# Kernel optimization log

Measured on AMD Instinct MI355X. Metric: run time of the kernel, lower is better.

Reference implementation:

```python
import jax, jax.numpy as jnp
import numpy as np

N = 100000
E = 1600000
IN_C = 64
HID = 64


def sage_conv(x, edge_index, W_l, b_l, W_r):
    # PyG SAGEConv with mean aggregation:
    # out = lin_l(mean_{j in N(i)} x_j) + lin_r(x_i)
    src, dst = edge_index[0], edge_index[1]
    msgs = x[src]                                        # [E, C] gather
    summed = jax.ops.segment_sum(msgs, dst, num_segments=N)   # [N, C]
    count = jax.ops.segment_sum(jnp.ones((edge_index.shape[1],), x.dtype), dst,
                                num_segments=N)          # [N]
    agg = summed / jnp.maximum(count, 1.0)[:, None]      # mean, safe for isolated nodes
    return agg @ W_l + b_l + x @ W_r


def setup_inputs() -> dict:
    key = jax.random.key(0)
    ks = jax.random.split(key, 10)
    x = jax.random.normal(ks[0], (N, IN_C), dtype=jnp.float32)
    edge_index = jax.random.randint(ks[1], (2, E), 0, N, dtype=jnp.int64)
    s1 = 1.0 / np.sqrt(IN_C)
    s2 = 1.0 / np.sqrt(HID)
    W_l1 = jax.random.uniform(ks[2], (IN_C, HID), jnp.float32, -s1, s1)
    b_l1 = jax.random.uniform(ks[3], (HID,), jnp.float32, -s1, s1)
    W_r1 = jax.random.uniform(ks[4], (IN_C, HID), jnp.float32, -s1, s1)
    W_l2 = jax.random.uniform(ks[5], (HID, HID), jnp.float32, -s2, s2)
    b_l2 = jax.random.uniform(ks[6], (HID,), jnp.float32, -s2, s2)
    W_r2 = jax.random.uniform(ks[7], (HID, HID), jnp.float32, -s2, s2)
    W_c = jax.random.uniform(ks[8], (HID, 1), jnp.float32, -s2, s2)
    b_c = jax.random.uniform(ks[9], (1,), jnp.float32, -s2, s2)
    return {"x": x, "edge_index": edge_index,
            "W_l1": W_l1, "b_l1": b_l1, "W_r1": W_r1,
            "W_l2": W_l2, "b_l2": b_l2, "W_r2": W_r2,
            "W_c": W_c, "b_c": b_c}


def reference(x, edge_index, W_l1, b_l1, W_r1, W_l2, b_l2, W_r2, W_c, b_c):
    h = jax.nn.relu(sage_conv(x, edge_index, W_l1, b_l1, W_r1))
    # dropout p=0.2 is identity in eval mode
    h = jax.nn.relu(sage_conv(h, edge_index, W_l2, b_l2, W_r2))
    out = (h @ W_c + b_c).squeeze(-1)   # [N]
    return out
```

## Files before the change

kernel.cpp:

```cpp
#include <hip/hip_runtime.h>


#define C 64
#define NB 196
#define BCAP 16000

typedef _Float16 half8 __attribute__((ext_vector_type(8)));
typedef float f32x4 __attribute__((ext_vector_type(4)));

static inline size_t align256(size_t x) { return (x + 255) & ~(size_t)255; }

__device__ void cvt_part(const float* __restrict__ x, _Float16* __restrict__ xh,
                         int n8, int bid) {
    int i = bid * 256 + (int)threadIdx.x;
    if (i < n8) {
        const float4* p = (const float4*)x + (size_t)i * 2;
        float4 a = p[0], b = p[1];
        half8 h;
        h[0] = (_Float16)a.x; h[1] = (_Float16)a.y; h[2] = (_Float16)a.z; h[3] = (_Float16)a.w;
        h[4] = (_Float16)b.x; h[5] = (_Float16)b.y; h[6] = (_Float16)b.z; h[7] = (_Float16)b.w;
        ((half8*)xh)[i] = h;
    }
}

__device__ void wpack_part(const float* __restrict__ W0, const float* __restrict__ W1,
                           const float* __restrict__ W2, const float* __restrict__ W3,
                           _Float16* __restrict__ wp, int bid) {
    int t = bid * 256 + (int)threadIdx.x;
    if (t >= 2048) return;
    int lane = t & 63, step = (t >> 6) & 1, tile = (t >> 7) & 3, mat = t >> 9;
    const float* W = (mat == 0) ? W0 : (mat == 1) ? W1 : (mat == 2) ? W2 : W3;
    int col = tile * 16 + (lane & 15);
    int k0  = step * 32 + ((lane >> 4) << 3);
    half8 h;
    #pragma unroll
    for (int j = 0; j < 8; ++j) h[j] = (_Float16)W[(k0 + j) * C + col];
    ((half8*)wp)[t] = h;
}

__global__ __launch_bounds__(256) void prep2_kernel(
    const float* __restrict__ x, _Float16* __restrict__ xh, int n8,
    const float* __restrict__ W0, const float* __restrict__ W1,
    const float* __restrict__ W2, const float* __restrict__ W3,
    _Float16* __restrict__ wp, int cgrid)
{
    int bid = blockIdx.x;
    if (bid < cgrid) cvt_part(x, xh, n8, bid);
    else             wpack_part(W0, W1, W2, W3, wp, bid - cgrid);
}

__global__ __launch_bounds__(256) void bucket1_kernel(
    const int* __restrict__ ei, int* __restrict__ bucketCnt,
    unsigned* __restrict__ records, int E)
{
    __shared__ int cnt[NB], cur[NB], gbase[NB];
    const int t = (int)threadIdx.x;
    for (int b = t; b < NB; b += 256) { cnt[b] = 0; cur[b] = 0; }
    __syncthreads();
    const int nE4 = E >> 2;
    const int base4 = blockIdx.x * 1024;
    #pragma unroll
    for (int j = 0; j < 4; ++j) {
        int i4 = base4 + j * 256 + t;
        if (i4 < nE4) {
            int4 d = ((const int4*)(ei + E))[i4];
            atomicAdd(&cnt[d.x >> 9], 1);
            atomicAdd(&cnt[d.y >> 9], 1);
            atomicAdd(&cnt[d.z >> 9], 1);
            atomicAdd(&cnt[d.w >> 9], 1);
        }
    }
    __syncthreads();
    for (int b = t; b < NB; b += 256)
        gbase[b] = cnt[b] ? atomicAdd(&bucketCnt[b], cnt[b]) : 0;
    __syncthreads();
    #pragma unroll
    for (int j = 0; j < 4; ++j) {
        int i4 = base4 + j * 256 + t;
        if (i4 < nE4) {
            int4 s = ((const int4*)ei)[i4];
            int4 d = ((const int4*)(ei + E))[i4];
            int b0 = d.x >> 9, b1 = d.y >> 9, b2 = d.z >> 9, b3 = d.w >> 9;
            int k0 = gbase[b0] + atomicAdd(&cur[b0], 1);
            int k1 = gbase[b1] + atomicAdd(&cur[b1], 1);
            int k2 = gbase[b2] + atomicAdd(&cur[b2], 1);
            int k3 = gbase[b3] + atomicAdd(&cur[b3], 1);
            if (k0 < BCAP) records[(size_t)b0 * BCAP + k0] = ((unsigned)s.x << 9) | (unsigned)(d.x & 511);
            if (k1 < BCAP) records[(size_t)b1 * BCAP + k1] = ((unsigned)s.y << 9) | (unsigned)(d.y & 511);
            if (k2 < BCAP) records[(size_t)b2 * BCAP + k2] = ((unsigned)s.z << 9) | (unsigned)(d.z & 511);
            if (k3 < BCAP) records[(size_t)b3 * BCAP + k3] = ((unsigned)s.w << 9) | (unsigned)(d.w & 511);
        }
    }
}

__global__ __launch_bounds__(256) void bucketscan_kernel(
    const int* __restrict__ bucketCnt, int* __restrict__ bucketBase,
    int* __restrict__ offs, int n)
{
    __shared__ int wsum[4];
    const int t = (int)threadIdx.x, lane = t & 63, wid = t >> 6;
    int v = (t < NB) ? min(bucketCnt[t], BCAP) : 0;
    int s = v;
    #pragma unroll
    for (int off = 1; off < 64; off <<= 1) {
        int u = __shfl_up(s, off, 64);
        if (lane >= off) s += u;
    }
    if (lane == 63) wsum[wid] = s;
    __syncthreads();
    int wpre = 0;
    for (int w = 0; w < wid; ++w) wpre += wsum[w];
    if (t < NB) bucketBase[t] = wpre + (s - v);
    if (t == 0) offs[n] = wsum[0] + wsum[1] + wsum[2] + wsum[3];
}

__global__ __launch_bounds__(256) void csrbuild_kernel(
    const unsigned* __restrict__ records, const int* __restrict__ bucketCnt,
    const int* __restrict__ bucketBase, int* __restrict__ offs,
    int* __restrict__ csr, int n)
{
    __shared__ int histo[512], cur[512], lofs[512], wsum[4];
    const int b = blockIdx.x, t = (int)threadIdx.x;
    const int cnt = min(bucketCnt[b], BCAP);
    const int bb = bucketBase[b];
    histo[t] = 0; histo[t + 256] = 0;
    cur[t] = 0;   cur[t + 256] = 0;
    __syncthreads();
    const unsigned* rec = records + (size_t)b * BCAP;
    for (int j = t; j < cnt; j += 256)
        atomicAdd(&histo[rec[j] & 511], 1);
    __syncthreads();
    int h0 = histo[2 * t], h1 = histo[2 * t + 1];
    int s = h0 + h1;
    const int lane = t & 63, wid = t >> 6;
    int si = s;
    #pragma unroll
    for (int off = 1; off < 64; off <<= 1) {
        int u = __shfl_up(si, off, 64);
        if (lane >= off) si += u;
    }
    if (lane == 63) wsum[wid] = si;
    __syncthreads();
    int wpre = 0;
    for (int w = 0; w < wid; ++w) wpre += wsum[w];
    int ex = wpre + (si - s);
    lofs[2 * t] = ex;
    lofs[2 * t + 1] = ex + h0;
    int node0 = b * 512 + 2 * t;
    if (node0 < n)     offs[node0]     = bb + ex;
    if (node0 + 1 < n) offs[node0 + 1] = bb + ex + h0;
    __syncthreads();
    for (int j = t; j < cnt; j += 256) {
        unsigned r = rec[j];
        int d = (int)(r & 511u);
        int rk = atomicAdd(&cur[d], 1);
        csr[bb + lofs[d] + rk] = (int)(r >> 9);
    }
}

template <bool FINAL>
__global__ __launch_bounds__(256) void sage_kernel(
    const _Float16* __restrict__ Xh, const int* __restrict__ csr,
    const int* __restrict__ offs,
    const _Float16* __restrict__ wpL, const _Float16* __restrict__ wpR,
    const float* __restrict__ bl,
    const float* __restrict__ Wc, const float* __restrict__ bc,
    void* __restrict__ outp, int n)
{
    const int lane = threadIdx.x & 63;
    const int wid  = threadIdx.x >> 6;
    const int base = blockIdx.x * 32;
    __shared__ _Float16 Aagg[32][72];
    __shared__ float Opart[2][2][16];

    const int slot = lane >> 3;
    const int sub  = lane & 7;
    const int node = base + wid * 8 + slot;
    float acc[8] = {0.f,0.f,0.f,0.f,0.f,0.f,0.f,0.f};
    int dcount = 0;
    if (node < n) {
        int start = offs[node];
        dcount = offs[node + 1] - start;
        int k = 0;
        for (; k + 4 <= dcount; k += 4) {
            int i0 = csr[start + k + 0];
            int i1 = csr[start + k + 1];
            int i2 = csr[start + k + 2];
            int i3 = csr[start + k + 3];
            half8 v0 = *(const half8*)(Xh + ((size_t)i0 << 6) + (sub << 3));
            half8 v1 = *(const half8*)(Xh + ((size_t)i1 << 6) + (sub << 3));
            half8 v2 = *(const half8*)(Xh + ((size_t)i2 << 6) + (sub << 3));
            half8 v3 = *(const half8*)(Xh + ((size_t)i3 << 6) + (sub << 3));
            #pragma unroll
            for (int j = 0; j < 8; ++j) acc[j] += (float)v0[j];
            #pragma unroll
            for (int j = 0; j < 8; ++j) acc[j] += (float)v1[j];
            #pragma unroll
            for (int j = 0; j < 8; ++j) acc[j] += (float)v2[j];
            #pragma unroll
            for (int j = 0; j < 8; ++j) acc[j] += (float)v3[j];
        }
        for (; k < dcount; ++k) {
            int i0 = csr[start + k];
            half8 v0 = *(const half8*)(Xh + ((size_t)i0 << 6) + (sub << 3));
            #pragma unroll
            for (int j = 0; j < 8; ++j) acc[j] += (float)v0[j];
        }
    }
    float inv = 1.0f / fmaxf((float)dcount, 1.0f);
    half8 hv;
    #pragma unroll
    for (int j = 0; j < 8; ++j) hv[j] = (_Float16)(acc[j] * inv);
    *(half8*)&Aagg[wid * 8 + slot][sub * 8] = hv;
    __syncthreads();

    const int Mtile = wid >> 1;
    const int pair  = wid & 1;
    const int row16 = lane & 15;
    const int kg    = lane >> 4;
    const int myrow = base + Mtile * 16 + row16;
    const int srow  = (myrow < n) ? myrow : 0;

    half8 ag0 = *(const half8*)&Aagg[Mtile * 16 + row16][kg * 8];
    half8 ag1 = *(const half8*)&Aagg[Mtile * 16 + row16][32 + kg * 8];
    const _Float16* xrow = Xh + ((size_t)srow << 6);
    half8 xi0 = *(const half8*)(xrow + kg * 8);
    half8 xi1 = *(const half8*)(xrow + 32 + kg * 8);

    float ptot[4] = {0.f, 0.f, 0.f, 0.f};
    #pragma unroll
    for (int q = 0; q < 2; ++q) {
        const int ct = pair * 2 + q;
        const half8* BL = (const half8*)(wpL + (size_t)ct * 1024);
        const half8* BR = (const half8*)(wpR + (size_t)ct * 1024);
        half8 b0 = BL[lane];
        half8 b1 = BL[64 + lane];
        half8 b2 = BR[lane];
        half8 b3 = BR[64 + lane];
        f32x4 cacc = {0.f, 0.f, 0.f, 0.f};
        cacc = __builtin_amdgcn_mfma_f32_16x16x32_f16(ag0, b0, cacc, 0, 0, 0);
        cacc = __builtin_amdgcn_mfma_f32_16x16x32_f16(ag1, b1, cacc, 0, 0, 0);
        cacc = __builtin_amdgcn_mfma_f32_16x16x32_f16(xi0, b2, cacc, 0, 0, 0);
        cacc = __builtin_amdgcn_mfma_f32_16x16x32_f16(xi1, b3, cacc, 0, 0, 0);

        const int col = ct * 16 + row16;
        const float bias = bl[col];
        if (!FINAL) {
            _Float16* h1 = (_Float16*)outp;
            #pragma unroll
            for (int j = 0; j < 4; ++j) {
                int r = base + Mtile * 16 + kg * 4 + j;
                if (r < n) {
                    float v = fmaxf(cacc[j] + bias, 0.f);
                    h1[((size_t)r << 6) + col] = (_Float16)v;
                }
            }
        } else {
            const float wc = Wc[col];
            float p[4];
            #pragma unroll
            for (int j = 0; j < 4; ++j) p[j] = fmaxf(cacc[j] + bias, 0.f) * wc;
            #pragma unroll
            for (int off = 1; off < 16; off <<= 1) {
                #pragma unroll
                for (int j = 0; j < 4; ++j) p[j] += __shfl_xor(p[j], off, 64);
            }
            #pragma unroll
            for (int j = 0; j < 4; ++j) ptot[j] += p[j];
        }
    }

    if (FINAL) {
        if (row16 == 0) {
            #pragma unroll
            for (int j = 0; j < 4; ++j) Opart[Mtile][pair][kg * 4 + j] = ptot[j];
        }
        __syncthreads();
        const int tid = threadIdx.x;
        if (tid < 32) {
            int Mt = tid >> 4, r = tid & 15;
            int gr = base + Mt * 16 + r;
            if (gr < n)
                ((float*)outp)[gr] = Opart[Mt][0][r] + Opart[Mt][1][r] + bc[0];
        }
    }
}

extern "C" void kernel_launch(void* const* d_in, const int* in_sizes, int n_in,
                              void* d_out, int out_size, void* d_ws, size_t ws_size,
                              hipStream_t stream) {
    const float* x   = (const float*)d_in[0];
    const int*   ei  = (const int*)d_in[1];
    const float* Wl1 = (const float*)d_in[2];
    const float* bl1 = (const float*)d_in[3];
    const float* Wr1 = (const float*)d_in[4];
    const float* Wl2 = (const float*)d_in[5];
    const float* bl2 = (const float*)d_in[6];
    const float* Wr2 = (const float*)d_in[7];
    const float* Wc  = (const float*)d_in[8];
    const float* bc  = (const float*)d_in[9];
    float* out = (float*)d_out;

    const int N = in_sizes[0] / C;
    const int E = in_sizes[1] / 2;

    char* ws = (char*)d_ws;
    size_t off = 0;
    int* offs       = (int*)(ws + off); off += align256((size_t)(N + 1) * 4);
    int* bucketCnt  = (int*)(ws + off); off += align256((size_t)NB * 4);
    int* bucketBase = (int*)(ws + off); off += align256((size_t)NB * 4);
    int* csr        = (int*)(ws + off); off += align256((size_t)E * 4);
    size_t h1_sz = (size_t)N * C * 2;
    size_t rec_sz = (size_t)NB * BCAP * 4;
    _Float16* h1 = (_Float16*)(ws + off); off += align256(h1_sz > rec_sz ? h1_sz : rec_sz);
    _Float16* xh = (_Float16*)(ws + off); off += align256((size_t)N * C * 2);
    _Float16* wp = (_Float16*)(ws + off); off += align256((size_t)2048 * 8 * 2);
    if (off > ws_size) return;

    unsigned* records = (unsigned*)h1;

    const int blk = 256;
    const int n8 = N * C / 8;
    const int cgrid = (n8 + blk - 1) / blk;
    const int nE4 = E >> 2;
    const int b1grid = (nE4 + 1023) / 1024;

    hipMemsetAsync(bucketCnt, 0, (size_t)NB * 4, stream);
    prep2_kernel<<<cgrid + 8, blk, 0, stream>>>(x, xh, n8, Wl1, Wr1, Wl2, Wr2, wp, cgrid);
    bucket1_kernel<<<b1grid, blk, 0, stream>>>(ei, bucketCnt, records, E);
    bucketscan_kernel<<<1, blk, 0, stream>>>(bucketCnt, bucketBase, offs, N);
    csrbuild_kernel<<<NB, blk, 0, stream>>>(records, bucketCnt, bucketBase, offs, csr, N);

    const int node_grid = (N + 31) / 32;
    sage_kernel<false><<<node_grid, blk, 0, stream>>>(
        xh, csr, offs, wp, wp + 4096, bl1, nullptr, nullptr, h1, N);
    sage_kernel<true><<<node_grid, blk, 0, stream>>>(
        h1, csr, offs, wp + 8192, wp + 12288, bl2, Wc, bc, out, N);
}
```

Before: 206.5 us.

## Fuse bucketing into prep kernel, fold bucket scan into CSR build, unroll gather by 8

Merges the edge-bucketing pass with the fp16 conversion and weight-packing blocks into one launch. The single-block bucket-offset scan is removed: each CSR-build block recomputes the prefix over all bucket counts itself. The destination indices are kept in registers between the count and scatter phases instead of being reloaded. The aggregation loop gains an 8-wide unrolled gather to keep more loads in flight, at the cost of register pressure and some redundant scan work in every CSR block.

```diff
diff --git a/kernel.cpp b/kernel.cpp
--- a/kernel.cpp
+++ b/kernel.cpp
@@ -9,6 +9,50 @@
 typedef float f32x4 __attribute__((ext_vector_type(4)));
 
 static inline size_t align256(size_t x) { return (x + 255) & ~(size_t)255; }
+
+__device__ void bucket1_part(const int* __restrict__ ei, int* __restrict__ bucketCnt,
+                             unsigned* __restrict__ records, int E, int bid) {
+    __shared__ int cnt[NB], cur[NB], gbase[NB];
+    const int t = (int)threadIdx.x;
+    for (int b = t; b < NB; b += 256) { cnt[b] = 0; cur[b] = 0; }
+    __syncthreads();
+    const int nE4 = E >> 2;
+    const int base4 = bid * 1024;
+    int4 dreg[4];
+    #pragma unroll
+    for (int j = 0; j < 4; ++j) {
+        int i4 = base4 + j * 256 + t;
+        if (i4 < nE4) {
+            int4 d = ((const int4*)(ei + E))[i4];
+            dreg[j] = d;
+            atomicAdd(&cnt[d.x >> 9], 1);
+            atomicAdd(&cnt[d.y >> 9], 1);
+            atomicAdd(&cnt[d.z >> 9], 1);
+            atomicAdd(&cnt[d.w >> 9], 1);
+        }
+    }
+    __syncthreads();
+    for (int b = t; b < NB; b += 256)
+        gbase[b] = cnt[b] ? atomicAdd(&bucketCnt[b], cnt[b]) : 0;
+    __syncthreads();
+    #pragma unroll
+    for (int j = 0; j < 4; ++j) {
+        int i4 = base4 + j * 256 + t;
+        if (i4 < nE4) {
+            int4 s = ((const int4*)ei)[i4];
+            int4 d = dreg[j];
+            int b0 = d.x >> 9, b1 = d.y >> 9, b2 = d.z >> 9, b3 = d.w >> 9;
+            int k0 = gbase[b0] + atomicAdd(&cur[b0], 1);
+            int k1 = gbase[b1] + atomicAdd(&cur[b1], 1);
+            int k2 = gbase[b2] + atomicAdd(&cur[b2], 1);
+            int k3 = gbase[b3] + atomicAdd(&cur[b3], 1);
+            if (k0 < BCAP) records[(size_t)b0 * BCAP + k0] = ((unsigned)s.x << 9) | (unsigned)(d.x & 511);
+            if (k1 < BCAP) records[(size_t)b1 * BCAP + k1] = ((unsigned)s.y << 9) | (unsigned)(d.y & 511);
+            if (k2 < BCAP) records[(size_t)b2 * BCAP + k2] = ((unsigned)s.z << 9) | (unsigned)(d.z & 511);
+            if (k3 < BCAP) records[(size_t)b3 * BCAP + k3] = ((unsigned)s.w << 9) | (unsigned)(d.w & 511);
+        }
+    }
+}
 
 __device__ void cvt_part(const float* __restrict__ x, _Float16* __restrict__ xh,
                          int n8, int bid) {
@@ -38,112 +82,65 @@
     ((half8*)wp)[t] = h;
 }
 
-__global__ __launch_bounds__(256) void prep2_kernel(
+__global__ __launch_bounds__(256) void prep_kernel(
+    const int* __restrict__ ei, int* __restrict__ bucketCnt,
+    unsigned* __restrict__ records, int E,
     const float* __restrict__ x, _Float16* __restrict__ xh, int n8,
     const float* __restrict__ W0, const float* __restrict__ W1,
     const float* __restrict__ W2, const float* __restrict__ W3,
-    _Float16* __restrict__ wp, int cgrid)
+    _Float16* __restrict__ wp, int bgrid, int cgrid)
 {
     int bid = blockIdx.x;
-    if (bid < cgrid) cvt_part(x, xh, n8, bid);
-    else             wpack_part(W0, W1, W2, W3, wp, bid - cgrid);
-}
-
-__global__ __launch_bounds__(256) void bucket1_kernel(
-    const int* __restrict__ ei, int* __restrict__ bucketCnt,
-    unsigned* __restrict__ records, int E)
+    if (bid < bgrid)              bucket1_part(ei, bucketCnt, records, E, bid);
+    else if (bid < bgrid + cgrid) cvt_part(x, xh, n8, bid - bgrid);
+    else                          wpack_part(W0, W1, W2, W3, wp, bid - bgrid - cgrid);
+}
+
+__global__ __launch_bounds__(256) void csrbuild_kernel(
+    const unsigned* __restrict__ records, const int* __restrict__ bucketCnt,
+    int* __restrict__ offs, int* __restrict__ csr, int n)
 {
-    __shared__ int cnt[NB], cur[NB], gbase[NB];
-    const int t = (int)threadIdx.x;
-    for (int b = t; b < NB; b += 256) { cnt[b] = 0; cur[b] = 0; }
-    __syncthreads();
-    const int nE4 = E >> 2;
-    const int base4 = blockIdx.x * 1024;
-    #pragma unroll
-    for (int j = 0; j < 4; ++j) {
-        int i4 = base4 + j * 256 + t;
-        if (i4 < nE4) {
-            int4 d = ((const int4*)(ei + E))[i4];
-            atomicAdd(&cnt[d.x >> 9], 1);
-            atomicAdd(&cnt[d.y >> 9], 1);
-            atomicAdd(&cnt[d.z >> 9], 1);
-            atomicAdd(&cnt[d.w >> 9], 1);
-        }
-    }
-    __syncthreads();
-    for (int b = t; b < NB; b += 256)
-        gbase[b] = cnt[b] ? atomicAdd(&bucketCnt[b], cnt[b]) : 0;
-    __syncthreads();
-    #pragma unroll
-    for (int j = 0; j < 4; ++j) {
-        int i4 = base4 + j * 256 + t;
-        if (i4 < nE4) {
-            int4 s = ((const int4*)ei)[i4];
-            int4 d = ((const int4*)(ei + E))[i4];
-            int b0 = d.x >> 9, b1 = d.y >> 9, b2 = d.z >> 9, b3 = d.w >> 9;
-            int k0 = gbase[b0] + atomicAdd(&cur[b0], 1);
-            int k1 = gbase[b1] + atomicAdd(&cur[b1], 1);
-            int k2 = gbase[b2] + atomicAdd(&cur[b2], 1);
-            int k3 = gbase[b3] + atomicAdd(&cur[b3], 1);
-            if (k0 < BCAP) records[(size_t)b0 * BCAP + k0] = ((unsigned)s.x << 9) | (unsigned)(d.x & 511);
-            if (k1 < BCAP) records[(size_t)b1 * BCAP + k1] = ((unsigned)s.y << 9) | (unsigned)(d.y & 511);
-            if (k2 < BCAP) records[(size_t)b2 * BCAP + k2] = ((unsigned)s.z << 9) | (unsigned)(d.z & 511);
-            if (k3 < BCAP) records[(size_t)b3 * BCAP + k3] = ((unsigned)s.w << 9) | (unsigned)(d.w & 511);
-        }
-    }
-}
-
-__global__ __launch_bounds__(256) void bucketscan_kernel(
-    const int* __restrict__ bucketCnt, int* __restrict__ bucketBase,
-    int* __restrict__ offs, int n)
-{
-    __shared__ int wsum[4];
-    const int t = (int)threadIdx.x, lane = t & 63, wid = t >> 6;
+    __shared__ int histo[512], cur[512], lofs[512], wsum[4];
+    __shared__ int bb_sh;
+    const int b = blockIdx.x, t = (int)threadIdx.x;
+    const int lane = t & 63, wid = t >> 6;
+    histo[t] = 0; histo[t + 256] = 0;
+    cur[t] = 0;   cur[t + 256] = 0;
     int v = (t < NB) ? min(bucketCnt[t], BCAP) : 0;
-    int s = v;
+    int si = v;
     #pragma unroll
     for (int off = 1; off < 64; off <<= 1) {
-        int u = __shfl_up(s, off, 64);
-        if (lane >= off) s += u;
-    }
-    if (lane == 63) wsum[wid] = s;
+        int u = __shfl_up(si, off, 64);
+        if (lane >= off) si += u;
+    }
+    if (lane == 63) wsum[wid] = si;
     __syncthreads();
     int wpre = 0;
     for (int w = 0; w < wid; ++w) wpre += wsum[w];
-    if (t < NB) bucketBase[t] = wpre + (s - v);
-    if (t == 0) offs[n] = wsum[0] + wsum[1] + wsum[2] + wsum[3];
-}
-
-__global__ __launch_bounds__(256) void csrbuild_kernel(
-    const unsigned* __restrict__ records, const int* __restrict__ bucketCnt,
-    const int* __restrict__ bucketBase, int* __restrict__ offs,
-    int* __restrict__ csr, int n)
-{
-    __shared__ int histo[512], cur[512], lofs[512], wsum[4];
-    const int b = blockIdx.x, t = (int)threadIdx.x;
+    if (t == b) bb_sh = wpre + (si - v);
+    if (b == 0 && t == 0)
+        offs[n] = wsum[0] + wsum[1] + wsum[2] + wsum[3];
+    __syncthreads();
     const int cnt = min(bucketCnt[b], BCAP);
-    const int bb = bucketBase[b];
-    histo[t] = 0; histo[t + 256] = 0;
-    cur[t] = 0;   cur[t + 256] = 0;
-    __syncthreads();
+    const int bb = bb_sh;
     const unsigned* rec = records + (size_t)b * BCAP;
     for (int j = t; j < cnt; j += 256)
         atomicAdd(&histo[rec[j] & 511], 1);
     __syncthreads();
     int h0 = histo[2 * t], h1 = histo[2 * t + 1];
     int s = h0 + h1;
-    const int lane = t & 63, wid = t >> 6;
-    int si = s;
+    int sj = s;
     #pragma unroll
     for (int off = 1; off < 64; off <<= 1) {
-        int u = __shfl_up(si, off, 64);
-        if (lane >= off) si += u;
-    }
-    if (lane == 63) wsum[wid] = si;
-    __syncthreads();
-    int wpre = 0;
-    for (int w = 0; w < wid; ++w) wpre += wsum[w];
-    int ex = wpre + (si - s);
+        int u = __shfl_up(sj, off, 64);
+        if (lane >= off) sj += u;
+    }
+    __syncthreads();
+    if (lane == 63) wsum[wid] = sj;
+    __syncthreads();
+    int wpre2 = 0;
+    for (int w = 0; w < wid; ++w) wpre2 += wsum[w];
+    int ex = wpre2 + (sj - s);
     lofs[2 * t] = ex;
     lofs[2 * t + 1] = ex + h0;
     int node0 = b * 512 + 2 * t;
@@ -182,6 +179,19 @@
         int start = offs[node];
         dcount = offs[node + 1] - start;
         int k = 0;
+        for (; k + 8 <= dcount; k += 8) {
+            int idx[8];
+            #pragma unroll
+            for (int jj = 0; jj < 8; ++jj) idx[jj] = csr[start + k + jj];
+            half8 v[8];
+            #pragma unroll
+            for (int jj = 0; jj < 8; ++jj)
+                v[jj] = *(const half8*)(Xh + ((size_t)idx[jj] << 6) + (sub << 3));
+            #pragma unroll
+            for (int jj = 0; jj < 8; ++jj)
+                #pragma unroll
+                for (int j = 0; j < 8; ++j) acc[j] += (float)v[jj][j];
+        }
         for (; k + 4 <= dcount; k += 4) {
             int i0 = csr[start + k + 0];
             int i1 = csr[start + k + 1];
@@ -306,10 +316,9 @@
 
     char* ws = (char*)d_ws;
     size_t off = 0;
-    int* offs       = (int*)(ws + off); off += align256((size_t)(N + 1) * 4);
-    int* bucketCnt  = (int*)(ws + off); off += align256((size_t)NB * 4);
-    int* bucketBase = (int*)(ws + off); off += align256((size_t)NB * 4);
-    int* csr        = (int*)(ws + off); off += align256((size_t)E * 4);
+    int* offs      = (int*)(ws + off); off += align256((size_t)(N + 1) * 4);
+    int* bucketCnt = (int*)(ws + off); off += align256((size_t)NB * 4);
+    int* csr       = (int*)(ws + off); off += align256((size_t)E * 4);
     size_t h1_sz = (size_t)N * C * 2;
     size_t rec_sz = (size_t)NB * BCAP * 4;
     _Float16* h1 = (_Float16*)(ws + off); off += align256(h1_sz > rec_sz ? h1_sz : rec_sz);
@@ -323,13 +332,12 @@
     const int n8 = N * C / 8;
     const int cgrid = (n8 + blk - 1) / blk;
     const int nE4 = E >> 2;
-    const int b1grid = (nE4 + 1023) / 1024;
+    const int bgrid = (nE4 + 1023) / 1024;
 
     hipMemsetAsync(bucketCnt, 0, (size_t)NB * 4, stream);
-    prep2_kernel<<<cgrid + 8, blk, 0, stream>>>(x, xh, n8, Wl1, Wr1, Wl2, Wr2, wp, cgrid);
-    bucket1_kernel<<<b1grid, blk, 0, stream>>>(ei, bucketCnt, records, E);
-    bucketscan_kernel<<<1, blk, 0, stream>>>(bucketCnt, bucketBase, offs, N);
-    csrbuild_kernel<<<NB, blk, 0, stream>>>(records, bucketCnt, bucketBase, offs, csr, N);
+    prep_kernel<<<bgrid + cgrid + 8, blk, 0, stream>>>(
+        ei, bucketCnt, records, E, x, xh, n8, Wl1, Wr1, Wl2, Wr2, wp, bgrid, cgrid);
+    csrbuild_kernel<<<NB, blk, 0, stream>>>(records, bucketCnt, offs, csr, N);
 
     const int node_grid = (N + 31) / 32;
     sage_kernel<false><<<node_grid, blk, 0, stream>>>(
```

Result: no change. 204.6 us (-0.9%).
